# Performance work log

Hardware: AMD Instinct MI355X
Metric: run time of the kernel (lower is better)

The kernel has to match this reference:

```python
import jax, jax.numpy as jnp
import numpy as np

B, T, C = 4, 2048, 1024
H, D = 16, 64
EPS = 1.1920929e-07  # torch.finfo(float32).eps, used by F.rms_norm default


def setup_inputs() -> dict:
    key = jax.random.key(0)
    ks = jax.random.split(key, 6)
    x = jax.random.normal(ks[0], (B, T, C), dtype=jnp.float32)
    # rotary cache: theta = 10000^(-2i/D), broadcastable [1, T, 1, D//2]
    inv_freq = 1.0 / (10000.0 ** (jnp.arange(0, D // 2, dtype=jnp.float32) * 2.0 / D))
    ang = jnp.arange(T, dtype=jnp.float32)[:, None] * inv_freq[None, :]  # [T, D//2]
    cos = jnp.cos(ang)[None, :, None, :]
    sin = jnp.sin(ang)[None, :, None, :]
    s = 0.02
    Wq = jax.random.normal(ks[1], (C, C), dtype=jnp.float32) * s
    Wk = jax.random.normal(ks[2], (C, C), dtype=jnp.float32) * s
    Wv = jax.random.normal(ks[3], (C, C), dtype=jnp.float32) * s
    Wo = jax.random.normal(ks[4], (C, C), dtype=jnp.float32) * s
    return {"x": x, "cos": cos, "sin": sin, "Wq": Wq, "Wk": Wk, "Wv": Wv, "Wo": Wo}


def _rope(x, cos, sin):
    d = x.shape[-1] // 2
    x1, x2 = x[..., :d], x[..., d:]
    return jnp.concatenate([x1 * cos + x2 * sin, -x1 * sin + x2 * cos], axis=-1)


def _rmsnorm(x):
    ms = jnp.mean(jnp.square(x), axis=-1, keepdims=True)
    return x * jax.lax.rsqrt(ms + EPS)


def reference(x, cos, sin, Wq, Wk, Wv, Wo):
    Bx, Tx, Cx = x.shape
    q = (x @ Wq.T).reshape(Bx, Tx, H, D)
    k = (x @ Wk.T).reshape(Bx, Tx, H, D)
    v = (x @ Wv.T).reshape(Bx, Tx, H, D)
    q = _rmsnorm(_rope(q, cos, sin))
    k = _rmsnorm(_rope(k, cos, sin))
    scale = 1.0 / jnp.sqrt(jnp.float32(D))
    # non-causal SDPA
    scores = jnp.einsum('bthd,bshd->bhts', q, k) * scale  # [B,H,T,T]
    attn = jax.nn.softmax(scores, axis=-1)
    y = jnp.einsum('bhts,bshd->bthd', attn, v).reshape(Bx, Tx, Cx)
    return y @ Wo.T
```

## Files before the change

### kernel.cpp

```cpp
#include <hip/hip_runtime.h>

#define B_ 4
#define T_ 2048
#define C_ 1024
#define H_ 16
#define D_ 64
#define EPS_ 1.1920929e-07f
#define LOG2E_ 1.4426950408889634f

typedef __attribute__((ext_vector_type(8))) short bf16x8;
typedef __attribute__((ext_vector_type(4))) float f32x4;
typedef unsigned short u16;
typedef unsigned int u32;

__device__ inline u16 f2bf(float f) {
  unsigned u = __float_as_uint(f);
  unsigned r = (u + 0x7fffu + ((u >> 16) & 1u)) >> 16;
  return (u16)r;
}

__device__ __forceinline__ void gload16(const void* g, void* l) {
  __builtin_amdgcn_global_load_lds(
      (__attribute__((address_space(1))) void*)g,
      (__attribute__((address_space(3))) void*)l, 16, 0, 0);
}

__global__ __launch_bounds__(256) void cvt_bf16(const float* __restrict__ src,
                                                u16* __restrict__ dst, int n) {
  const int i = (blockIdx.x * 256 + threadIdx.x) * 4;
  if (i < n) {
    float4 v = *(const float4*)&src[i];
    ushort4 o;
    o.x = f2bf(v.x); o.y = f2bf(v.y); o.z = f2bf(v.z); o.w = f2bf(v.w);
    *(ushort4*)&dst[i] = o;
  }
}

__global__ __launch_bounds__(256) void cvt_weights(const float* __restrict__ wq,
                                                   const float* __restrict__ wk,
                                                   const float* __restrict__ wv,
                                                   const float* __restrict__ wo,
                                                   u16* __restrict__ wqkv,
                                                   u16* __restrict__ wob, int n) {
  const int i = (blockIdx.x * 256 + threadIdx.x) * 4;
  const int t = blockIdx.y;
  const float* src = (t == 0) ? wq : (t == 1) ? wk : (t == 2) ? wv : wo;
  u16* dst = (t == 3) ? wob : (wqkv + (size_t)t * n);
  if (i < n) {
    float4 v = *(const float4*)&src[i];
    ushort4 o;
    o.x = f2bf(v.x); o.y = f2bf(v.y); o.z = f2bf(v.z); o.w = f2bf(v.w);
    *(ushort4*)&dst[i] = o;
  }
}

__global__ __launch_bounds__(256) void gemm_qkv(const u16* __restrict__ X,
                                                const u16* __restrict__ W,
                                                u16* __restrict__ qb,
                                                u16* __restrict__ kb,
                                                u16* __restrict__ vtb,
                                                const float* __restrict__ cs,
                                                const float* __restrict__ sn,
                                                int M, int K) {
  __shared__ short As[128 * 64];
  __shared__ short Bs[128 * 64];
  const int tid = threadIdx.x;
  const int lane = tid & 63;
  const int w = tid >> 6;
  const int wr = w >> 1, wc = w & 1;
  const int m0 = blockIdx.y * 128, n0 = blockIdx.x * 128;
  const int lrow = lane >> 3;
  const int lcol = (lane & 7) * 8;

  f32x4 acc[4][4];
#pragma unroll
  for (int mi = 0; mi < 4; ++mi)
#pragma unroll
    for (int ni = 0; ni < 4; ++ni)
      acc[mi][ni] = (f32x4){0.f, 0.f, 0.f, 0.f};

  const int r = lane & 15;
  const int quad = lane >> 4;

  for (int kt = 0; kt < K; kt += 64) {
#pragma unroll
    for (int i = 0; i < 4; ++i) {
      const int row = w * 32 + i * 8;
      gload16(&X[(size_t)(m0 + row + lrow) * K + kt + lcol], &As[row * 64]);
      gload16(&W[(size_t)(n0 + row + lrow) * K + kt + lcol], &Bs[row * 64]);
    }
    __syncthreads();
#pragma unroll
    for (int kc = 0; kc < 2; ++kc) {
      const int ko = kc * 32 + quad * 8;
      bf16x8 a[4], b[4];
#pragma unroll
      for (int mi = 0; mi < 4; ++mi)
        a[mi] = *(const bf16x8*)&As[(wr * 64 + mi * 16 + r) * 64 + ko];
#pragma unroll
      for (int ni = 0; ni < 4; ++ni)
        b[ni] = *(const bf16x8*)&Bs[(wc * 64 + ni * 16 + r) * 64 + ko];
#pragma unroll
      for (int mi = 0; mi < 4; ++mi)
#pragma unroll
        for (int ni = 0; ni < 4; ++ni)
          acc[mi][ni] = __builtin_amdgcn_mfma_f32_16x16x32_bf16(a[mi], b[ni], acc[mi][ni], 0, 0, 0);
    }
    __syncthreads();
  }

  const int which = blockIdx.x >> 3;
  const int c0 = (blockIdx.x & 7) * 128 + wc * 64;

  if (which < 2) {
    u16* dst = (which == 0) ? qb : kb;
#pragma unroll
    for (int mi = 0; mi < 4; ++mi)
#pragma unroll
      for (int j = 0; j < 4; ++j) {
        const int gr = m0 + wr * 64 + mi * 16 + quad * 4 + j;
        const int t = gr & (T_ - 1);
        float o[4];
#pragma unroll
        for (int ni = 0; ni < 2; ++ni) {
          const float c = cs[t * 32 + ni * 16 + r];
          const float s = sn[t * 32 + ni * 16 + r];
          const float x1 = acc[mi][ni][j], x2 = acc[mi][ni + 2][j];
          o[ni]     = x1 * c + x2 * s;
          o[ni + 2] = x2 * c - x1 * s;
        }
        float sq = o[0] * o[0] + o[1] * o[1] + o[2] * o[2] + o[3] * o[3];
        sq += __shfl_xor(sq, 1, 64);
        sq += __shfl_xor(sq, 2, 64);
        sq += __shfl_xor(sq, 4, 64);
        sq += __shfl_xor(sq, 8, 64);
        float rn = rsqrtf(sq * (1.0f / 64.0f) + EPS_);
        if (which == 0) rn *= 0.125f * LOG2E_;
#pragma unroll
        for (int ni = 0; ni < 4; ++ni)
          dst[(size_t)gr * C_ + c0 + ni * 16 + r] = f2bf(o[ni] * rn);
      }
  } else {
    const int h = (blockIdx.x & 7) * 2 + wc;
    const int gr0 = m0 + wr * 64;
    const int bb = gr0 >> 11;
    const int tbase = gr0 & (T_ - 1);
#pragma unroll
    for (int ni = 0; ni < 4; ++ni) {
      const int d = ni * 16 + r;
      bf16x8 o0, o1;
#pragma unroll
      for (int mi = 0; mi < 4; ++mi)
#pragma unroll
        for (int j = 0; j < 4; ++j) {
          const int idx = j * 4 + mi;
          const u16 vv = f2bf(acc[mi][ni][j]);
          if (idx < 8) o0[idx] = (short)vv; else o1[idx - 8] = (short)vv;
        }
      u16* p = &vtb[((size_t)((bb * H_ + h) * D_ + d)) * T_ + tbase + quad * 16];
      *(bf16x8*)&p[0] = o0;
      *(bf16x8*)&p[8] = o1;
    }
  }
}

__global__ __launch_bounds__(256) void gemm_out(const u16* __restrict__ X,
                                                const u16* __restrict__ W,
                                                float* __restrict__ Y,
                                                int M, int N, int K) {
  __shared__ short As[128 * 64];
  __shared__ short Bs[128 * 64];
  const int tid = threadIdx.x;
  const int lane = tid & 63;
  const int w = tid >> 6;
  const int wr = w >> 1, wc = w & 1;
  const int m0 = blockIdx.y * 128, n0 = blockIdx.x * 128;
  const int lrow = lane >> 3;
  const int lcol = (lane & 7) * 8;

  f32x4 acc[4][4];
#pragma unroll
  for (int mi = 0; mi < 4; ++mi)
#pragma unroll
    for (int ni = 0; ni < 4; ++ni)
      acc[mi][ni] = (f32x4){0.f, 0.f, 0.f, 0.f};

  const int r = lane & 15;
  const int quad = lane >> 4;

  for (int kt = 0; kt < K; kt += 64) {
#pragma unroll
    for (int i = 0; i < 4; ++i) {
      const int row = w * 32 + i * 8;
      gload16(&X[(size_t)(m0 + row + lrow) * K + kt + lcol], &As[row * 64]);
      gload16(&W[(size_t)(n0 + row + lrow) * K + kt + lcol], &Bs[row * 64]);
    }
    __syncthreads();
#pragma unroll
    for (int kc = 0; kc < 2; ++kc) {
      const int ko = kc * 32 + quad * 8;
      bf16x8 a[4], b[4];
#pragma unroll
      for (int mi = 0; mi < 4; ++mi)
        a[mi] = *(const bf16x8*)&As[(wr * 64 + mi * 16 + r) * 64 + ko];
#pragma unroll
      for (int ni = 0; ni < 4; ++ni)
        b[ni] = *(const bf16x8*)&Bs[(wc * 64 + ni * 16 + r) * 64 + ko];
#pragma unroll
      for (int mi = 0; mi < 4; ++mi)
#pragma unroll
        for (int ni = 0; ni < 4; ++ni)
          acc[mi][ni] = __builtin_amdgcn_mfma_f32_16x16x32_bf16(a[mi], b[ni], acc[mi][ni], 0, 0, 0);
    }
    __syncthreads();
  }

#pragma unroll
  for (int mi = 0; mi < 4; ++mi)
#pragma unroll
    for (int ni = 0; ni < 4; ++ni) {
      const int gc = n0 + wc * 64 + ni * 16 + r;
#pragma unroll
      for (int j = 0; j < 4; ++j) {
        const int gr = m0 + wr * 64 + mi * 16 + quad * 4 + j;
        Y[(size_t)gr * N + gc] = acc[mi][ni][j];
      }
    }
}

__global__ __launch_bounds__(256) void flash_mfma(const u16* __restrict__ Qb,
                                                  const u16* __restrict__ Kb,
                                                  const u16* __restrict__ Vtb,
                                                  u16* __restrict__ Yb) {
  __shared__ u16 Ks[64][72];
  __shared__ u16 Vt[64][72];
  __shared__ u16 Ps[128][72];
  const int tid = threadIdx.x;
  const int lane = tid & 63;
  const int w = tid >> 6;
  const int r = lane & 15;
  const int quad = lane >> 4;
  const int bh = blockIdx.x, qt = blockIdx.y;
  const int b = bh >> 4, h = bh & 15;
  const int srow = lane;
  const int sd0 = w * 16;
  const int vrow = tid >> 2;
  const int vco = (tid & 3) * 16;

  {
    const int row = tid >> 1, half = tid & 1;
    const size_t g = ((size_t)((b * T_ + qt * 128 + row) * H_ + h)) * D_ + half * 32;
    *(bf16x8*)&Ps[row][half * 32]      = *(const bf16x8*)&Qb[g];
    *(bf16x8*)&Ps[row][half * 32 + 8]  = *(const bf16x8*)&Qb[g + 8];
    *(bf16x8*)&Ps[row][half * 32 + 16] = *(const bf16x8*)&Qb[g + 16];
    *(bf16x8*)&Ps[row][half * 32 + 24] = *(const bf16x8*)&Qb[g + 24];
  }
  __syncthreads();
  bf16x8 qf[2][2];
#pragma unroll
  for (int qg = 0; qg < 2; ++qg)
#pragma unroll
    for (int kc = 0; kc < 2; ++kc)
      qf[qg][kc] = *(const bf16x8*)&Ps[w * 32 + qg * 16 + r][kc * 32 + quad * 8];

  f32x4 oacc[2][4];
#pragma unroll
  for (int qg = 0; qg < 2; ++qg)
#pragma unroll
    for (int ni = 0; ni < 4; ++ni) oacc[qg][ni] = (f32x4){0.f, 0.f, 0.f, 0.f};
  float l_i[2][4];
#pragma unroll
  for (int qg = 0; qg < 2; ++qg)
#pragma unroll
    for (int j = 0; j < 4; ++j) l_i[qg][j] = 0.f;

  bf16x8 k0, k1, v0, v1;
  {
    const size_t gk = ((size_t)((b * T_ + srow) * H_ + h)) * D_ + sd0;
    k0 = *(const bf16x8*)&Kb[gk];
    k1 = *(const bf16x8*)&Kb[gk + 8];
    const size_t gv = ((size_t)(bh * 64 + vrow)) * T_ + vco;
    v0 = *(const bf16x8*)&Vtb[gv];
    v1 = *(const bf16x8*)&Vtb[gv + 8];
  }

  for (int kt = 0; kt < T_; kt += 64) {
    *(bf16x8*)&Ks[srow][sd0] = k0;
    *(bf16x8*)&Ks[srow][sd0 + 8] = k1;
    *(bf16x8*)&Vt[vrow][vco] = v0;
    *(bf16x8*)&Vt[vrow][vco + 8] = v1;
    __syncthreads();
    if (kt + 64 < T_) {
      const size_t gk = ((size_t)((b * T_ + kt + 64 + srow) * H_ + h)) * D_ + sd0;
      k0 = *(const bf16x8*)&Kb[gk];
      k1 = *(const bf16x8*)&Kb[gk + 8];
      const size_t gv = ((size_t)(bh * 64 + vrow)) * T_ + kt + 64 + vco;
      v0 = *(const bf16x8*)&Vtb[gv];
      v1 = *(const bf16x8*)&Vtb[gv + 8];
    }

    f32x4 s[2][4];
#pragma unroll
    for (int qg = 0; qg < 2; ++qg)
#pragma unroll
      for (int ni = 0; ni < 4; ++ni) s[qg][ni] = (f32x4){0.f, 0.f, 0.f, 0.f};
#pragma unroll
    for (int ni = 0; ni < 4; ++ni)
#pragma unroll
      for (int kc = 0; kc < 2; ++kc) {
        bf16x8 kf = *(const bf16x8*)&Ks[ni * 16 + r][kc * 32 + quad * 8];
        s[0][ni] = __builtin_amdgcn_mfma_f32_16x16x32_bf16(qf[0][kc], kf, s[0][ni], 0, 0, 0);
        s[1][ni] = __builtin_amdgcn_mfma_f32_16x16x32_bf16(qf[1][kc], kf, s[1][ni], 0, 0, 0);
      }

#pragma unroll
    for (int qg = 0; qg < 2; ++qg)
#pragma unroll
      for (int j = 0; j < 4; ++j) {
        const float p0 = __builtin_amdgcn_exp2f(s[qg][0][j]);
        const float p1 = __builtin_amdgcn_exp2f(s[qg][1][j]);
        const float p2 = __builtin_amdgcn_exp2f(s[qg][2][j]);
        const float p3 = __builtin_amdgcn_exp2f(s[qg][3][j]);
        l_i[qg][j] += (p0 + p1) + (p2 + p3);
        u32 lo, hi;
        asm("v_cvt_pk_bf16_f32 %0, %1, %2" : "=v"(lo) : "v"(p0), "v"(p1));
        asm("v_cvt_pk_bf16_f32 %0, %1, %2" : "=v"(hi) : "v"(p2), "v"(p3));
        const int prow = w * 32 + qg * 16 + quad * 4 + j;
        *(uint2*)&Ps[prow][r * 4] = make_uint2(lo, hi);
      }

#pragma unroll
    for (int kc = 0; kc < 2; ++kc) {
      bf16x8 vf[4];
#pragma unroll
      for (int ni = 0; ni < 4; ++ni)
        vf[ni] = *(const bf16x8*)&Vt[ni * 16 + r][kc * 32 + quad * 8];
#pragma unroll
      for (int qg = 0; qg < 2; ++qg) {
        bf16x8 pf = *(const bf16x8*)&Ps[w * 32 + qg * 16 + r][kc * 32 + quad * 8];
#pragma unroll
        for (int ni = 0; ni < 4; ++ni)
          oacc[qg][ni] = __builtin_amdgcn_mfma_f32_16x16x32_bf16(pf, vf[ni], oacc[qg][ni], 0, 0, 0);
      }
    }
    __syncthreads();
  }

#pragma unroll
  for (int qg = 0; qg < 2; ++qg)
#pragma unroll
    for (int j = 0; j < 4; ++j) {
      float l = l_i[qg][j];
      l += __shfl_xor(l, 1, 64);
      l += __shfl_xor(l, 2, 64);
      l += __shfl_xor(l, 4, 64);
      l += __shfl_xor(l, 8, 64);
      const float inv = 1.0f / l;
      const int t = qt * 128 + w * 32 + qg * 16 + quad * 4 + j;
      const size_t gbase = ((size_t)((b * T_ + t) * H_ + h)) * D_;
#pragma unroll
      for (int ni = 0; ni < 4; ++ni)
        Yb[gbase + ni * 16 + r] = f2bf(oacc[qg][ni][j] * inv);
    }
}

extern "C" void kernel_launch(void* const* d_in, const int* in_sizes, int n_in,
                              void* d_out, int out_size, void* d_ws, size_t ws_size,
                              hipStream_t stream) {
  const float* x    = (const float*)d_in[0];
  const float* cosb = (const float*)d_in[1];
  const float* sinb = (const float*)d_in[2];
  const float* Wq   = (const float*)d_in[3];
  const float* Wk   = (const float*)d_in[4];
  const float* Wv   = (const float*)d_in[5];
  const float* Wo   = (const float*)d_in[6];
  float* out = (float*)d_out;

  const size_t NE = (size_t)B_ * T_ * C_;
  const int CC = C_ * C_;
  u16* xb   = (u16*)d_ws;
  u16* qb   = xb + NE;
  u16* kb   = qb + NE;
  u16* vtb  = kb + NE;
  u16* wqkv = vtb + NE;
  u16* wob  = wqkv + 3 * (size_t)CC;
  u16* yb   = xb;

  const int M = B_ * T_;

  cvt_bf16<<<(int)(NE / 1024), 256, 0, stream>>>(x, xb, (int)NE);
  dim3 wg(CC / 1024, 4);
  cvt_weights<<<wg, 256, 0, stream>>>(Wq, Wk, Wv, Wo, wqkv, wob, CC);

  dim3 qg(24, M / 128), gb(256);
  gemm_qkv<<<qg, gb, 0, stream>>>(xb, wqkv, qb, kb, vtb, cosb, sinb, M, C_);

  dim3 fg(B_ * H_, T_ / 128);
  flash_mfma<<<fg, 256, 0, stream>>>(qb, kb, vtb, yb);

  dim3 og(C_ / 128, M / 128);
  gemm_out<<<og, gb, 0, stream>>>(yb, wob, out, M, C_, C_);
}
```

Measured before the change: 309.1 us.

## Rewrite flash attention with 32x32 MFMA, register-resident P and double-buffered K/V

The attention kernel moves from 16x16x32 to 32x32x16 bf16 MFMA and computes S transposed (K as the A operand), so each lane holds one query column. P is packed to bf16 and rearranged across half-waves with v_permlane32_swap instead of going through an LDS round trip. K/V tiles are double-buffered in LDS with a two-tile-ahead register prefetch. The V-transpose epilogue of the QKV GEMM also switches to packed bf16 conversion with narrower stores. These changes aim to cut LDS traffic and synchronisation in the inner loop, at the cost of tricky lane mapping that must be exactly right.

```diff
diff --git a/kernel.cpp b/kernel.cpp
--- a/kernel.cpp
+++ b/kernel.cpp
@@ -10,8 +10,10 @@
 
 typedef __attribute__((ext_vector_type(8))) short bf16x8;
 typedef __attribute__((ext_vector_type(4))) float f32x4;
+typedef __attribute__((ext_vector_type(16))) float f32x16;
 typedef unsigned short u16;
 typedef unsigned int u32;
+typedef __attribute__((ext_vector_type(4))) u32 u32x4;
 
 __device__ inline u16 f2bf(float f) {
   unsigned u = __float_as_uint(f);
@@ -148,18 +150,16 @@
 #pragma unroll
     for (int ni = 0; ni < 4; ++ni) {
       const int d = ni * 16 + r;
-      bf16x8 o0, o1;
-#pragma unroll
-      for (int mi = 0; mi < 4; ++mi)
-#pragma unroll
-        for (int j = 0; j < 4; ++j) {
-          const int idx = j * 4 + mi;
-          const u16 vv = f2bf(acc[mi][ni][j]);
-          if (idx < 8) o0[idx] = (short)vv; else o1[idx - 8] = (short)vv;
-        }
-      u16* p = &vtb[((size_t)((bb * H_ + h) * D_ + d)) * T_ + tbase + quad * 16];
-      *(bf16x8*)&p[0] = o0;
-      *(bf16x8*)&p[8] = o1;
+      u16* rowp = &vtb[((size_t)((bb * H_ + h) * D_ + d)) * T_ + tbase];
+#pragma unroll
+      for (int mi = 0; mi < 4; ++mi) {
+        u32 lo, hi2;
+        asm("v_cvt_pk_bf16_f32 %0, %1, %2" : "=v"(lo) : "v"(acc[mi][ni][0]), "v"(acc[mi][ni][1]));
+        asm("v_cvt_pk_bf16_f32 %0, %1, %2" : "=v"(hi2) : "v"(acc[mi][ni][2]), "v"(acc[mi][ni][3]));
+        u16* p = rowp + mi * 16 + quad * 2;
+        *(u32*)&p[0] = lo;
+        *(u32*)&p[8] = hi2;
+      }
     }
   }
 }
@@ -232,47 +232,19 @@
                                                   const u16* __restrict__ Kb,
                                                   const u16* __restrict__ Vtb,
                                                   u16* __restrict__ Yb) {
-  __shared__ u16 Ks[64][72];
-  __shared__ u16 Vt[64][72];
-  __shared__ u16 Ps[128][72];
+  __shared__ u16 Ks[2][64][72];
+  __shared__ u16 Vt[2][64][72];
   const int tid = threadIdx.x;
   const int lane = tid & 63;
   const int w = tid >> 6;
-  const int r = lane & 15;
-  const int quad = lane >> 4;
+  const int c = lane & 31;
+  const int hi = lane >> 5;
   const int bh = blockIdx.x, qt = blockIdx.y;
   const int b = bh >> 4, h = bh & 15;
   const int srow = lane;
   const int sd0 = w * 16;
   const int vrow = tid >> 2;
   const int vco = (tid & 3) * 16;
-
-  {
-    const int row = tid >> 1, half = tid & 1;
-    const size_t g = ((size_t)((b * T_ + qt * 128 + row) * H_ + h)) * D_ + half * 32;
-    *(bf16x8*)&Ps[row][half * 32]      = *(const bf16x8*)&Qb[g];
-    *(bf16x8*)&Ps[row][half * 32 + 8]  = *(const bf16x8*)&Qb[g + 8];
-    *(bf16x8*)&Ps[row][half * 32 + 16] = *(const bf16x8*)&Qb[g + 16];
-    *(bf16x8*)&Ps[row][half * 32 + 24] = *(const bf16x8*)&Qb[g + 24];
-  }
-  __syncthreads();
-  bf16x8 qf[2][2];
-#pragma unroll
-  for (int qg = 0; qg < 2; ++qg)
-#pragma unroll
-    for (int kc = 0; kc < 2; ++kc)
-      qf[qg][kc] = *(const bf16x8*)&Ps[w * 32 + qg * 16 + r][kc * 32 + quad * 8];
-
-  f32x4 oacc[2][4];
-#pragma unroll
-  for (int qg = 0; qg < 2; ++qg)
-#pragma unroll
-    for (int ni = 0; ni < 4; ++ni) oacc[qg][ni] = (f32x4){0.f, 0.f, 0.f, 0.f};
-  float l_i[2][4];
-#pragma unroll
-  for (int qg = 0; qg < 2; ++qg)
-#pragma unroll
-    for (int j = 0; j < 4; ++j) l_i[qg][j] = 0.f;
 
   bf16x8 k0, k1, v0, v1;
   {
@@ -284,84 +256,119 @@
     v1 = *(const bf16x8*)&Vtb[gv + 8];
   }
 
-  for (int kt = 0; kt < T_; kt += 64) {
-    *(bf16x8*)&Ks[srow][sd0] = k0;
-    *(bf16x8*)&Ks[srow][sd0 + 8] = k1;
-    *(bf16x8*)&Vt[vrow][vco] = v0;
-    *(bf16x8*)&Vt[vrow][vco + 8] = v1;
+  {
+    const int row = tid >> 1, half = tid & 1;
+    const size_t g = ((size_t)((b * T_ + qt * 128 + row) * H_ + h)) * D_ + half * 32;
+    u16* qd = (row < 64) ? &Ks[0][row][half * 32] : &Ks[1][row - 64][half * 32];
+    *(bf16x8*)&qd[0]  = *(const bf16x8*)&Qb[g];
+    *(bf16x8*)&qd[8]  = *(const bf16x8*)&Qb[g + 8];
+    *(bf16x8*)&qd[16] = *(const bf16x8*)&Qb[g + 16];
+    *(bf16x8*)&qd[24] = *(const bf16x8*)&Qb[g + 24];
+  }
+  __syncthreads();
+  bf16x8 qf[4];
+  {
+    const int qr = w * 32 + c;
+    const u16* qs = (qr < 64) ? &Ks[0][qr][0] : &Ks[1][qr - 64][0];
+#pragma unroll
+    for (int ks = 0; ks < 4; ++ks)
+      qf[ks] = *(const bf16x8*)&qs[ks * 16 + hi * 8];
+  }
+  __syncthreads();
+
+  *(bf16x8*)&Ks[0][srow][sd0] = k0;
+  *(bf16x8*)&Ks[0][srow][sd0 + 8] = k1;
+  *(bf16x8*)&Vt[0][vrow][vco] = v0;
+  *(bf16x8*)&Vt[0][vrow][vco + 8] = v1;
+  {
+    const size_t gk = ((size_t)((b * T_ + 64 + srow) * H_ + h)) * D_ + sd0;
+    k0 = *(const bf16x8*)&Kb[gk];
+    k1 = *(const bf16x8*)&Kb[gk + 8];
+    const size_t gv = ((size_t)(bh * 64 + vrow)) * T_ + 64 + vco;
+    v0 = *(const bf16x8*)&Vtb[gv];
+    v1 = *(const bf16x8*)&Vtb[gv + 8];
+  }
+  __syncthreads();
+
+  f32x16 oacc[2];
+  oacc[0] = (f32x16)(0.f);
+  oacc[1] = (f32x16)(0.f);
+  float l_acc = 0.f;
+
+  const int NT = T_ / 64;
+  for (int t = 0; t < NT; ++t) {
+    const int cur = t & 1;
+
+    f32x16 s0 = (f32x16)(0.f), s1 = (f32x16)(0.f);
+#pragma unroll
+    for (int ks = 0; ks < 4; ++ks) {
+      bf16x8 kf0 = *(const bf16x8*)&Ks[cur][c][ks * 16 + hi * 8];
+      bf16x8 kf1 = *(const bf16x8*)&Ks[cur][32 + c][ks * 16 + hi * 8];
+      s0 = __builtin_amdgcn_mfma_f32_32x32x16_bf16(kf0, qf[ks], s0, 0, 0, 0);
+      s1 = __builtin_amdgcn_mfma_f32_32x32x16_bf16(kf1, qf[ks], s1, 0, 0, 0);
+    }
+
+    if (t + 1 < NT) {
+      const int nxt = cur ^ 1;
+      *(bf16x8*)&Ks[nxt][srow][sd0] = k0;
+      *(bf16x8*)&Ks[nxt][srow][sd0 + 8] = k1;
+      *(bf16x8*)&Vt[nxt][vrow][vco] = v0;
+      *(bf16x8*)&Vt[nxt][vrow][vco + 8] = v1;
+      if (t + 2 < NT) {
+        const size_t gk = ((size_t)((b * T_ + (t + 2) * 64 + srow) * H_ + h)) * D_ + sd0;
+        k0 = *(const bf16x8*)&Kb[gk];
+        k1 = *(const bf16x8*)&Kb[gk + 8];
+        const size_t gv = ((size_t)(bh * 64 + vrow)) * T_ + (t + 2) * 64 + vco;
+        v0 = *(const bf16x8*)&Vtb[gv];
+        v1 = *(const bf16x8*)&Vtb[gv + 8];
+      }
+    }
+
+    u32 wrd[2][4][2];
+#pragma unroll
+    for (int m = 0; m < 4; ++m)
+#pragma unroll
+      for (int p = 0; p < 2; ++p) {
+        float a0 = __builtin_amdgcn_exp2f(s0[m * 4 + p * 2]);
+        float a1 = __builtin_amdgcn_exp2f(s0[m * 4 + p * 2 + 1]);
+        float b0 = __builtin_amdgcn_exp2f(s1[m * 4 + p * 2]);
+        float b1 = __builtin_amdgcn_exp2f(s1[m * 4 + p * 2 + 1]);
+        l_acc += (a0 + a1) + (b0 + b1);
+        asm("v_cvt_pk_bf16_f32 %0, %1, %2" : "=v"(wrd[0][m][p]) : "v"(a0), "v"(a1));
+        asm("v_cvt_pk_bf16_f32 %0, %1, %2" : "=v"(wrd[1][m][p]) : "v"(b0), "v"(b1));
+      }
+#pragma unroll
+    for (int kt2 = 0; kt2 < 2; ++kt2)
+#pragma unroll
+      for (int m = 0; m < 4; ++m)
+        asm("v_permlane32_swap_b32 %0, %1" : "+v"(wrd[kt2][m][0]), "+v"(wrd[kt2][m][1]));
+
+    bf16x8 pa[4];
+    pa[0] = __builtin_bit_cast(bf16x8, (u32x4){wrd[0][0][0], wrd[0][0][1], wrd[0][1][0], wrd[0][1][1]});
+    pa[1] = __builtin_bit_cast(bf16x8, (u32x4){wrd[0][2][0], wrd[0][2][1], wrd[0][3][0], wrd[0][3][1]});
+    pa[2] = __builtin_bit_cast(bf16x8, (u32x4){wrd[1][0][0], wrd[1][0][1], wrd[1][1][0], wrd[1][1][1]});
+    pa[3] = __builtin_bit_cast(bf16x8, (u32x4){wrd[1][2][0], wrd[1][2][1], wrd[1][3][0], wrd[1][3][1]});
+
+#pragma unroll
+    for (int ks = 0; ks < 4; ++ks) {
+      bf16x8 vf0 = *(const bf16x8*)&Vt[cur][c][ks * 16 + hi * 8];
+      bf16x8 vf1 = *(const bf16x8*)&Vt[cur][32 + c][ks * 16 + hi * 8];
+      oacc[0] = __builtin_amdgcn_mfma_f32_32x32x16_bf16(pa[ks], vf0, oacc[0], 0, 0, 0);
+      oacc[1] = __builtin_amdgcn_mfma_f32_32x32x16_bf16(pa[ks], vf1, oacc[1], 0, 0, 0);
+    }
     __syncthreads();
-    if (kt + 64 < T_) {
-      const size_t gk = ((size_t)((b * T_ + kt + 64 + srow) * H_ + h)) * D_ + sd0;
-      k0 = *(const bf16x8*)&Kb[gk];
-      k1 = *(const bf16x8*)&Kb[gk + 8];
-      const size_t gv = ((size_t)(bh * 64 + vrow)) * T_ + kt + 64 + vco;
-      v0 = *(const bf16x8*)&Vtb[gv];
-      v1 = *(const bf16x8*)&Vtb[gv + 8];
-    }
-
-    f32x4 s[2][4];
-#pragma unroll
-    for (int qg = 0; qg < 2; ++qg)
-#pragma unroll
-      for (int ni = 0; ni < 4; ++ni) s[qg][ni] = (f32x4){0.f, 0.f, 0.f, 0.f};
-#pragma unroll
-    for (int ni = 0; ni < 4; ++ni)
-#pragma unroll
-      for (int kc = 0; kc < 2; ++kc) {
-        bf16x8 kf = *(const bf16x8*)&Ks[ni * 16 + r][kc * 32 + quad * 8];
-        s[0][ni] = __builtin_amdgcn_mfma_f32_16x16x32_bf16(qf[0][kc], kf, s[0][ni], 0, 0, 0);
-        s[1][ni] = __builtin_amdgcn_mfma_f32_16x16x32_bf16(qf[1][kc], kf, s[1][ni], 0, 0, 0);
-      }
-
-#pragma unroll
-    for (int qg = 0; qg < 2; ++qg)
-#pragma unroll
-      for (int j = 0; j < 4; ++j) {
-        const float p0 = __builtin_amdgcn_exp2f(s[qg][0][j]);
-        const float p1 = __builtin_amdgcn_exp2f(s[qg][1][j]);
-        const float p2 = __builtin_amdgcn_exp2f(s[qg][2][j]);
-        const float p3 = __builtin_amdgcn_exp2f(s[qg][3][j]);
-        l_i[qg][j] += (p0 + p1) + (p2 + p3);
-        u32 lo, hi;
-        asm("v_cvt_pk_bf16_f32 %0, %1, %2" : "=v"(lo) : "v"(p0), "v"(p1));
-        asm("v_cvt_pk_bf16_f32 %0, %1, %2" : "=v"(hi) : "v"(p2), "v"(p3));
-        const int prow = w * 32 + qg * 16 + quad * 4 + j;
-        *(uint2*)&Ps[prow][r * 4] = make_uint2(lo, hi);
-      }
-
-#pragma unroll
-    for (int kc = 0; kc < 2; ++kc) {
-      bf16x8 vf[4];
-#pragma unroll
-      for (int ni = 0; ni < 4; ++ni)
-        vf[ni] = *(const bf16x8*)&Vt[ni * 16 + r][kc * 32 + quad * 8];
-#pragma unroll
-      for (int qg = 0; qg < 2; ++qg) {
-        bf16x8 pf = *(const bf16x8*)&Ps[w * 32 + qg * 16 + r][kc * 32 + quad * 8];
-#pragma unroll
-        for (int ni = 0; ni < 4; ++ni)
-          oacc[qg][ni] = __builtin_amdgcn_mfma_f32_16x16x32_bf16(pf, vf[ni], oacc[qg][ni], 0, 0, 0);
-      }
-    }
-    __syncthreads();
-  }
-
-#pragma unroll
-  for (int qg = 0; qg < 2; ++qg)
-#pragma unroll
-    for (int j = 0; j < 4; ++j) {
-      float l = l_i[qg][j];
-      l += __shfl_xor(l, 1, 64);
-      l += __shfl_xor(l, 2, 64);
-      l += __shfl_xor(l, 4, 64);
-      l += __shfl_xor(l, 8, 64);
-      const float inv = 1.0f / l;
-      const int t = qt * 128 + w * 32 + qg * 16 + quad * 4 + j;
-      const size_t gbase = ((size_t)((b * T_ + t) * H_ + h)) * D_;
-#pragma unroll
-      for (int ni = 0; ni < 4; ++ni)
-        Yb[gbase + ni * 16 + r] = f2bf(oacc[qg][ni][j] * inv);
-    }
+  }
+
+  float l_all = l_acc + __shfl_xor(l_acc, 32, 64);
+#pragma unroll
+  for (int v = 0; v < 16; ++v) {
+    const int q = (v & 3) + 8 * (v >> 2) + 4 * hi;
+    const float inv = 1.0f / __shfl(l_all, q, 64);
+    const int tq = qt * 128 + w * 32 + q;
+    const size_t gbase = ((size_t)((b * T_ + tq) * H_ + h)) * D_;
+    Yb[gbase + c]      = f2bf(oacc[0][v] * inv);
+    Yb[gbase + 32 + c] = f2bf(oacc[1][v] * inv);
+  }
 }
 
 extern "C" void kernel_launch(void* const* d_in, const int* in_sizes, int n_in,
```

New measurement: 312.9 us. Within noise of the previous version (+1.2%).
